# Performance work log

Hardware: AMD Instinct MI355X
Metric: run time of the kernel (lower is better)

The kernel has to match this reference:

```python
import jax, jax.numpy as jnp
import numpy as np
import math

D_MODEL = 1024
N_HEADS = 16
HEAD_DIM = 64


def setup_inputs() -> dict:
    key = jax.random.key(0)
    k_x, k_q, k_k, k_v, k_o = jax.random.split(key, 5)
    lecun = jax.nn.initializers.lecun_normal()
    return {
        "x": jax.random.normal(k_x, (4, 2048, D_MODEL), dtype=jnp.float32),
        "W_q": lecun(k_q, (N_HEADS, D_MODEL, HEAD_DIM), jnp.float32),
        "W_k": lecun(k_k, (N_HEADS, D_MODEL, HEAD_DIM), jnp.float32),
        "W_v": lecun(k_v, (N_HEADS, D_MODEL, HEAD_DIM), jnp.float32),
        "W_o": lecun(k_o, (D_MODEL, D_MODEL), jnp.float32),
    }


def reference(x, W_q, W_k, W_v, W_o):
    # x: [b, l, e]; W_{q,k,v}: [h, e, d]; W_o: [e, e]
    q = jnp.einsum('ble,hed->bhld', x, W_q)
    k = jnp.einsum('ble,hed->bhld', x, W_k)
    v = jnp.einsum('ble,hed->bhld', x, W_v)
    scores = jnp.einsum('bhld,bhsd->bhls', q, k) / math.sqrt(HEAD_DIM)
    attn = jax.nn.softmax(scores, axis=-1)
    av = jnp.einsum('bhls,bhsd->bhld', attn, v)  # [b, h, l, d]
    b, h, l, d = av.shape
    concat = jnp.transpose(av, (0, 2, 1, 3)).reshape(b, l, h * d)
    out = jnp.einsum('ble,eo->blo', concat, W_o)
    return jnp.asarray(out, dtype=jnp.float32)
```

## Files before the change

kernel.cpp:

```cpp
#include <hip/hip_runtime.h>

#define BATCH 4
#define LSEQ  2048
#define DM    1024
#define NH    16
#define HD    64
#define NTOK  (BATCH * LSEQ)

typedef _Float16 f16x8 __attribute__((ext_vector_type(8)));
typedef _Float16 f16x4 __attribute__((ext_vector_type(4)));
typedef __fp16   hf16x2 __attribute__((ext_vector_type(2)));
typedef float    f32x4 __attribute__((ext_vector_type(4)));

typedef __attribute__((address_space(1))) const unsigned int GU32;
typedef __attribute__((address_space(3))) unsigned int LU32;

__device__ __forceinline__ void gload_lds16(const _Float16* g, _Float16* l)
{
    __builtin_amdgcn_global_load_lds(
        (GU32*)(unsigned long long)g,
        (LU32*)(unsigned int)(unsigned long long)l, 16, 0, 0);
}


__global__ __launch_bounds__(256) void cvt_kernel(const float* __restrict__ src,
                                                  _Float16* __restrict__ dst, int n4)
{
    int i = blockIdx.x * 256 + threadIdx.x;
    if (i >= n4) return;
    float4 v = ((const float4*)src)[i];
    f16x4 h;
    h[0] = (_Float16)v.x; h[1] = (_Float16)v.y; h[2] = (_Float16)v.z; h[3] = (_Float16)v.w;
    ((f16x4*)dst)[i] = h;
}

__global__ __launch_bounds__(256) void tconv3_kernel(
    const float* __restrict__ Wq, const float* __restrict__ Wk,
    const float* __restrict__ Wv, _Float16* __restrict__ dst)
{
    const int z = blockIdx.z;
    const int which = z >> 4, h = z & 15;
    const float* __restrict__ src =
        ((which == 0) ? Wq : (which == 1) ? Wk : Wv) + (size_t)h * DM * HD;
    _Float16* __restrict__ d = dst + (size_t)z * DM * HD;
    const int e0 = blockIdx.y * 64;
    __shared__ float Ls[64][65];
    const int t = threadIdx.x;
    #pragma unroll
    for (int j = 0; j < 4; ++j) {
        int cidx = t + j * 256;
        int row = cidx >> 4, col4 = (cidx & 15) * 4;
        float4 v = *(const float4*)&src[(size_t)(e0 + row) * HD + col4];
        Ls[row][col4] = v.x; Ls[row][col4+1] = v.y; Ls[row][col4+2] = v.z; Ls[row][col4+3] = v.w;
    }
    __syncthreads();
    const int dd = t & 63, sc = t >> 6;
    alignas(16) _Float16 tmp[16];
    #pragma unroll
    for (int i = 0; i < 16; ++i) tmp[i] = (_Float16)Ls[sc * 16 + i][dd];
    *(f16x8*)&d[(size_t)dd * DM + e0 + sc * 16]     = *(f16x8*)&tmp[0];
    *(f16x8*)&d[(size_t)dd * DM + e0 + sc * 16 + 8] = *(f16x8*)&tmp[8];
}

__global__ __launch_bounds__(256) void tconv_kernel(const float* __restrict__ src,
                                                    _Float16* __restrict__ dst, int E, int D)
{
    const int d0 = blockIdx.x * 64, e0 = blockIdx.y * 64;
    __shared__ float Ls[64][65];
    const int t = threadIdx.x;
    #pragma unroll
    for (int j = 0; j < 4; ++j) {
        int cidx = t + j * 256;
        int row = cidx >> 4, col4 = (cidx & 15) * 4;
        float4 v = *(const float4*)&src[(size_t)(e0 + row) * D + d0 + col4];
        Ls[row][col4] = v.x; Ls[row][col4+1] = v.y; Ls[row][col4+2] = v.z; Ls[row][col4+3] = v.w;
    }
    __syncthreads();
    const int dd = t & 63, sc = t >> 6;
    alignas(16) _Float16 tmp[16];
    #pragma unroll
    for (int i = 0; i < 16; ++i) tmp[i] = (_Float16)Ls[sc * 16 + i][dd];
    *(f16x8*)&dst[(size_t)(d0 + dd) * E + e0 + sc * 16]     = *(f16x8*)&tmp[0];
    *(f16x8*)&dst[(size_t)(d0 + dd) * E + e0 + sc * 16 + 8] = *(f16x8*)&tmp[8];
}

template<int MODE>
__global__ __launch_bounds__(256) void gemm_kernel(
    const _Float16* __restrict__ A, const _Float16* __restrict__ B,
    float* __restrict__ out32,
    _Float16* __restrict__ qo, _Float16* __restrict__ ko, _Float16* __restrict__ vto)
{
    const int n0 = blockIdx.x * 128, m0 = blockIdx.y * 128;
    __shared__ _Float16 As[128 * 64];
    __shared__ _Float16 Bs[128 * 64];
    const int t = threadIdx.x;
    const int lane = t & 63, w = t >> 6;
    const int quad = lane >> 4, c = lane & 15;
    const int wm = (w & 1) * 64, wn = (w >> 1) * 64;
    const int srow = lane >> 3;
    const int scol8 = ((lane & 7) ^ (lane >> 3)) * 8;

    const int colsw = (quad ^ (c & 7)) * 8;
    const _Float16* Ap0 = &As[(wm + c) * 64 + colsw];
    const _Float16* Ap1 = &As[(wm + c) * 64 + (colsw ^ 32)];
    const _Float16* Bp0 = &Bs[(wn + c) * 64 + colsw];
    const _Float16* Bp1 = &Bs[(wn + c) * 64 + (colsw ^ 32)];

    f32x4 acc[4][4];
    #pragma unroll
    for (int i = 0; i < 4; ++i)
        #pragma unroll
        for (int j = 0; j < 4; ++j) acc[i][j] = {0.f, 0.f, 0.f, 0.f};

    for (int e0 = 0; e0 < DM; e0 += 64) {
        __syncthreads();
        #pragma unroll
        for (int j = 0; j < 4; ++j) {
            int ch = w * 4 + j;
            gload_lds16(A + (size_t)(m0 + ch * 8 + srow) * DM + e0 + scol8, As + ch * 512);
            gload_lds16(B + (size_t)(n0 + ch * 8 + srow) * DM + e0 + scol8, Bs + ch * 512);
        }
        __syncthreads();
        #pragma unroll
        for (int kc = 0; kc < 2; ++kc) {
            const _Float16* Ap = kc ? Ap1 : Ap0;
            const _Float16* Bp = kc ? Bp1 : Bp0;
            f16x8 af[4], bf[4];
            #pragma unroll
            for (int mt = 0; mt < 4; ++mt) af[mt] = *(const f16x8*)(Ap + mt * 1024);
            #pragma unroll
            for (int nt = 0; nt < 4; ++nt) bf[nt] = *(const f16x8*)(Bp + nt * 1024);
            #pragma unroll
            for (int mt = 0; mt < 4; ++mt)
                #pragma unroll
                for (int nt = 0; nt < 4; ++nt)
                    acc[mt][nt] = __builtin_amdgcn_mfma_f32_16x16x32_f16(af[mt], bf[nt], acc[mt][nt], 0, 0, 0);
        }
    }

    if (MODE == 0) {
        #pragma unroll
        for (int mt = 0; mt < 4; ++mt)
            #pragma unroll
            for (int nt = 0; nt < 4; ++nt)
                #pragma unroll
                for (int r = 0; r < 4; ++r) {
                    int row = m0 + wm + mt * 16 + quad * 4 + r;
                    int col = n0 + wn + nt * 16 + c;
                    out32[(size_t)row * DM + col] = acc[mt][nt][r];
                }
    } else {
        const int mi = (n0 + wn) >> 6;
        const int which = mi >> 4, hh = mi & 15;
        if (which == 2) {
            #pragma unroll
            for (int mt = 0; mt < 4; ++mt) {
                int tok0 = m0 + wm + mt * 16 + quad * 4;
                int b = tok0 >> 11, l = tok0 & (LSEQ - 1);
                #pragma unroll
                for (int nt = 0; nt < 4; ++nt) {
                    int d = nt * 16 + c;
                    f16x4 pk;
                    pk[0] = (_Float16)acc[mt][nt][0];
                    pk[1] = (_Float16)acc[mt][nt][1];
                    pk[2] = (_Float16)acc[mt][nt][2];
                    pk[3] = (_Float16)acc[mt][nt][3];
                    *(f16x4*)&vto[((size_t)(b * NH + hh) * HD + d) * LSEQ + l] = pk;
                }
            }
        } else {
            _Float16* dst = (which == 0) ? qo : ko;
            const float vs = (which == 0) ? 0.18033688011112042f : 1.0f;
            #pragma unroll
            for (int mt = 0; mt < 4; ++mt)
                #pragma unroll
                for (int nt = 0; nt < 4; ++nt)
                    #pragma unroll
                    for (int r = 0; r < 4; ++r) {
                        int tok = m0 + wm + mt * 16 + quad * 4 + r;
                        int b = tok >> 11, l = tok & (LSEQ - 1);
                        int d = nt * 16 + c;
                        dst[((size_t)(b * NH + hh) * LSEQ + l) * HD + d] = (_Float16)(acc[mt][nt][r] * vs);
                    }
        }
    }
}

__global__ __launch_bounds__(256, 3) void attn_kernel(
    const _Float16* __restrict__ Qg, const _Float16* __restrict__ Kg,
    const _Float16* __restrict__ Vtg, _Float16* __restrict__ concat)
{
    const int bh = blockIdx.x;
    const int q0 = blockIdx.y * 128;
    const int b = bh >> 4, h = bh & (NH - 1);
    __shared__ _Float16 Ks[2][64 * 64];
    __shared__ _Float16 Vts[2][64 * 64];
    __shared__ _Float16 Ps[4][32][72];
    const int t = threadIdx.x;
    const int lane = t & 63, w = t >> 6;
    const int quad = lane >> 4, c = lane & 15;
    const int srow = lane >> 3;
    const int scol8 = ((lane & 7) ^ (lane >> 3)) * 8;

    const int colsw = (quad ^ (c & 7)) * 8;
    const int kOffA = c * 64 + colsw;
    const int kOffB = c * 64 + (colsw ^ 32);
    _Float16*       PsW = &Ps[w][c][quad * 4];
    const _Float16* PsR = &Ps[w][c][quad * 8];

    f16x8 qf[2][2];
    #pragma unroll
    for (int mi = 0; mi < 2; ++mi)
        #pragma unroll
        for (int kc = 0; kc < 2; ++kc)
            qf[mi][kc] = *(const f16x8*)&Qg[((size_t)bh * LSEQ + q0 + w * 32 + mi * 16 + c) * HD + kc * 32 + quad * 8];

    f32x4 o[2][4];
    #pragma unroll
    for (int mi = 0; mi < 2; ++mi)
        #pragma unroll
        for (int dt = 0; dt < 4; ++dt) o[mi][dt] = {0.f, 0.f, 0.f, 0.f};
    float lp[2] = {0.f, 0.f};

    auto stage = [&](int bi, int s0n) {
        #pragma unroll
        for (int j = 0; j < 2; ++j) {
            int ch = w * 2 + j;
            gload_lds16(Kg  + ((size_t)bh * LSEQ + s0n + ch * 8 + srow) * HD + scol8, &Ks[bi][ch * 512]);
            gload_lds16(Vtg + ((size_t)bh * HD + ch * 8 + srow) * LSEQ + s0n + scol8, &Vts[bi][ch * 512]);
        }
    };

    constexpr int NT = LSEQ / 64;
    stage(0, 0);
    int cur = 0;

    for (int tt = 0; tt < NT; ++tt) {
        if (tt + 1 < NT) {
            stage(cur ^ 1, (tt + 1) * 64);
            asm volatile("s_waitcnt vmcnt(4)" ::: "memory");
        } else {
            asm volatile("s_waitcnt vmcnt(0)" ::: "memory");
        }
        __builtin_amdgcn_s_barrier();
        __builtin_amdgcn_sched_barrier(0);

        const _Float16* Kb = &Ks[cur][0];
        const _Float16* Vb = &Vts[cur][0];

        #pragma unroll
        for (int st = 0; st < 4; ++st) {
            f32x4 sT[2];
            #pragma unroll
            for (int mi = 0; mi < 2; ++mi) sT[mi] = {0.f, 0.f, 0.f, 0.f};
            #pragma unroll
            for (int kc = 0; kc < 2; ++kc) {
                f16x8 kf = *(const f16x8*)(Kb + (kc ? kOffB : kOffA) + st * 1024);
                #pragma unroll
                for (int mi = 0; mi < 2; ++mi)
                    sT[mi] = __builtin_amdgcn_mfma_f32_16x16x32_f16(kf, qf[mi][kc], sT[mi], 0, 0, 0);
            }
            #pragma unroll
            for (int mi = 0; mi < 2; ++mi) {
                float p0 = __builtin_amdgcn_exp2f(sT[mi][0]);
                float p1 = __builtin_amdgcn_exp2f(sT[mi][1]);
                float p2 = __builtin_amdgcn_exp2f(sT[mi][2]);
                float p3 = __builtin_amdgcn_exp2f(sT[mi][3]);
                lp[mi] += (p0 + p1) + (p2 + p3);
                union { hf16x2 h2[2]; f16x4 h4; } u;
                u.h2[0] = __builtin_amdgcn_cvt_pkrtz(p0, p1);
                u.h2[1] = __builtin_amdgcn_cvt_pkrtz(p2, p3);
                *(f16x4*)(PsW + mi * 1152 + st * 16) = u.h4;
            }
        }

        #pragma unroll
        for (int sc = 0; sc < 2; ++sc) {
            f16x8 pf[2];
            #pragma unroll
            for (int mi = 0; mi < 2; ++mi)
                pf[mi] = *(const f16x8*)(PsR + mi * 1152 + sc * 32);
            #pragma unroll
            for (int dt = 0; dt < 4; ++dt) {
                f16x8 vf = *(const f16x8*)(Vb + (sc ? kOffB : kOffA) + dt * 1024);
                #pragma unroll
                for (int mi = 0; mi < 2; ++mi)
                    o[mi][dt] = __builtin_amdgcn_mfma_f32_16x16x32_f16(pf[mi], vf, o[mi][dt], 0, 0, 0);
            }
        }

        __builtin_amdgcn_s_barrier();
        cur ^= 1;
    }

    #pragma unroll
    for (int mi = 0; mi < 2; ++mi) {
        lp[mi] += __shfl_xor(lp[mi], 16);
        lp[mi] += __shfl_xor(lp[mi], 32);
    }

    #pragma unroll
    for (int mi = 0; mi < 2; ++mi)
        #pragma unroll
        for (int r = 0; r < 4; ++r) {
            float inv = 1.f / __shfl(lp[mi], quad * 4 + r);
            int row = q0 + w * 32 + mi * 16 + quad * 4 + r;
            #pragma unroll
            for (int dt = 0; dt < 4; ++dt)
                concat[((size_t)b * LSEQ + row) * DM + h * HD + dt * 16 + c] =
                    (_Float16)(o[mi][dt][r] * inv);
        }
}

extern "C" void kernel_launch(void* const* d_in, const int* in_sizes, int n_in,
                              void* d_out, int out_size, void* d_ws, size_t ws_size,
                              hipStream_t stream)
{
    (void)in_sizes; (void)n_in; (void)out_size; (void)ws_size;

    const float* x  = (const float*)d_in[0];
    const float* Wq = (const float*)d_in[1];
    const float* Wk = (const float*)d_in[2];
    const float* Wv = (const float*)d_in[3];
    const float* Wo = (const float*)d_in[4];
    float* out = (float*)d_out;

    const size_t XE = (size_t)NTOK * DM;
    const size_t WQKV = (size_t)3 * NH * HD * DM;
    _Float16* xh  = (_Float16*)d_ws;
    _Float16* WtA = xh + XE;
    _Float16* Wot = WtA + WQKV;
    _Float16* q   = Wot + (size_t)DM * DM;
    _Float16* k   = q + XE;
    _Float16* vt  = k + XE;
    _Float16* cc  = vt + XE;

    cvt_kernel<<<8192, 256, 0, stream>>>(x, xh, (int)(XE / 4));
    tconv3_kernel<<<dim3(1, 16, 48), 256, 0, stream>>>(Wq, Wk, Wv, WtA);
    tconv_kernel<<<dim3(16, 16, 1), 256, 0, stream>>>(Wo, Wot, DM, DM);

    gemm_kernel<1><<<dim3(24, 64), 256, 0, stream>>>(xh, WtA, nullptr, q, k, vt);
    attn_kernel<<<dim3(64, LSEQ / 128), 256, 0, stream>>>(q, k, vt, cc);
    gemm_kernel<0><<<dim3(8, 64), 256, 0, stream>>>(cc, Wot, out, nullptr, nullptr, nullptr);
}
```

Before: 280.2 us.

## Switch attention to 32x32x16 MFMA and keep P in registers

```diff
diff --git a/kernel.cpp b/kernel.cpp
--- a/kernel.cpp
+++ b/kernel.cpp
@@ -11,6 +11,7 @@
 typedef _Float16 f16x4 __attribute__((ext_vector_type(4)));
 typedef __fp16   hf16x2 __attribute__((ext_vector_type(2)));
 typedef float    f32x4 __attribute__((ext_vector_type(4)));
+typedef float    f32x16 __attribute__((ext_vector_type(16)));
 
 typedef __attribute__((address_space(1))) const unsigned int GU32;
 typedef __attribute__((address_space(3))) unsigned int LU32;
@@ -186,41 +187,30 @@
     }
 }
 
-__global__ __launch_bounds__(256, 3) void attn_kernel(
+__global__ __launch_bounds__(256, 4) void attn_kernel(
     const _Float16* __restrict__ Qg, const _Float16* __restrict__ Kg,
     const _Float16* __restrict__ Vtg, _Float16* __restrict__ concat)
 {
     const int bh = blockIdx.x;
     const int q0 = blockIdx.y * 128;
-    const int b = bh >> 4, h = bh & (NH - 1);
+    const int b = bh >> 4, head = bh & (NH - 1);
     __shared__ _Float16 Ks[2][64 * 64];
     __shared__ _Float16 Vts[2][64 * 64];
-    __shared__ _Float16 Ps[4][32][72];
     const int t = threadIdx.x;
     const int lane = t & 63, w = t >> 6;
-    const int quad = lane >> 4, c = lane & 15;
+    const int m = lane & 31, hl = lane >> 5;
     const int srow = lane >> 3;
     const int scol8 = ((lane & 7) ^ (lane >> 3)) * 8;
 
-    const int colsw = (quad ^ (c & 7)) * 8;
-    const int kOffA = c * 64 + colsw;
-    const int kOffB = c * 64 + (colsw ^ 32);
-    _Float16*       PsW = &Ps[w][c][quad * 4];
-    const _Float16* PsR = &Ps[w][c][quad * 8];
-
-    f16x8 qf[2][2];
-    #pragma unroll
-    for (int mi = 0; mi < 2; ++mi)
-        #pragma unroll
-        for (int kc = 0; kc < 2; ++kc)
-            qf[mi][kc] = *(const f16x8*)&Qg[((size_t)bh * LSEQ + q0 + w * 32 + mi * 16 + c) * HD + kc * 32 + quad * 8];
-
-    f32x4 o[2][4];
-    #pragma unroll
-    for (int mi = 0; mi < 2; ++mi)
-        #pragma unroll
-        for (int dt = 0; dt < 4; ++dt) o[mi][dt] = {0.f, 0.f, 0.f, 0.f};
-    float lp[2] = {0.f, 0.f};
+    f16x8 qf[4];
+    #pragma unroll
+    for (int kstep = 0; kstep < 4; ++kstep)
+        qf[kstep] = *(const f16x8*)&Qg[((size_t)bh * LSEQ + q0 + w * 32 + m) * HD + kstep * 16 + hl * 8];
+
+    f32x16 o[2];
+    #pragma unroll
+    for (int i = 0; i < 16; ++i) { o[0][i] = 0.f; o[1][i] = 0.f; }
+    float lp = 0.f;
 
     auto stage = [&](int bi, int s0n) {
         #pragma unroll
@@ -248,68 +238,65 @@
         const _Float16* Kb = &Ks[cur][0];
         const _Float16* Vb = &Vts[cur][0];
 
-        #pragma unroll
-        for (int st = 0; st < 4; ++st) {
-            f32x4 sT[2];
-            #pragma unroll
-            for (int mi = 0; mi < 2; ++mi) sT[mi] = {0.f, 0.f, 0.f, 0.f};
-            #pragma unroll
-            for (int kc = 0; kc < 2; ++kc) {
-                f16x8 kf = *(const f16x8*)(Kb + (kc ? kOffB : kOffA) + st * 1024);
-                #pragma unroll
-                for (int mi = 0; mi < 2; ++mi)
-                    sT[mi] = __builtin_amdgcn_mfma_f32_16x16x32_f16(kf, qf[mi][kc], sT[mi], 0, 0, 0);
+        f16x8 pf[4];
+        #pragma unroll
+        for (int sblk = 0; sblk < 2; ++sblk) {
+            const int rr = sblk * 32 + m;
+            const int rx = rr & 7;
+            const _Float16* Krow = Kb + rr * 64;
+            f32x16 sT;
+            #pragma unroll
+            for (int i = 0; i < 16; ++i) sT[i] = 0.f;
+            #pragma unroll
+            for (int kstep = 0; kstep < 4; ++kstep) {
+                f16x8 kf = *(const f16x8*)(Krow + (((kstep * 2 + hl) ^ rx) * 8));
+                sT = __builtin_amdgcn_mfma_f32_32x32x16_f16(kf, qf[kstep], sT, 0, 0, 0);
             }
-            #pragma unroll
-            for (int mi = 0; mi < 2; ++mi) {
-                float p0 = __builtin_amdgcn_exp2f(sT[mi][0]);
-                float p1 = __builtin_amdgcn_exp2f(sT[mi][1]);
-                float p2 = __builtin_amdgcn_exp2f(sT[mi][2]);
-                float p3 = __builtin_amdgcn_exp2f(sT[mi][3]);
-                lp[mi] += (p0 + p1) + (p2 + p3);
-                union { hf16x2 h2[2]; f16x4 h4; } u;
-                u.h2[0] = __builtin_amdgcn_cvt_pkrtz(p0, p1);
-                u.h2[1] = __builtin_amdgcn_cvt_pkrtz(p2, p3);
-                *(f16x4*)(PsW + mi * 1152 + st * 16) = u.h4;
+            union { unsigned int u[4]; f16x8 v; } P0, P1;
+            #pragma unroll
+            for (int q = 0; q < 8; ++q) {
+                float e0 = __builtin_amdgcn_exp2f(sT[2 * q]);
+                float e1 = __builtin_amdgcn_exp2f(sT[2 * q + 1]);
+                lp += e0 + e1;
+                union { hf16x2 h; unsigned int u; } uu;
+                uu.h = __builtin_amdgcn_cvt_pkrtz(e0, e1);
+                if (q < 4) P0.u[q] = uu.u; else P1.u[q - 4] = uu.u;
             }
-        }
-
-        #pragma unroll
-        for (int sc = 0; sc < 2; ++sc) {
-            f16x8 pf[2];
-            #pragma unroll
-            for (int mi = 0; mi < 2; ++mi)
-                pf[mi] = *(const f16x8*)(PsR + mi * 1152 + sc * 32);
-            #pragma unroll
-            for (int dt = 0; dt < 4; ++dt) {
-                f16x8 vf = *(const f16x8*)(Vb + (sc ? kOffB : kOffA) + dt * 1024);
-                #pragma unroll
-                for (int mi = 0; mi < 2; ++mi)
-                    o[mi][dt] = __builtin_amdgcn_mfma_f32_16x16x32_f16(pf[mi], vf, o[mi][dt], 0, 0, 0);
+            pf[sblk * 2 + 0] = P0.v;
+            pf[sblk * 2 + 1] = P1.v;
+        }
+
+        #pragma unroll
+        for (int dblk = 0; dblk < 2; ++dblk) {
+            const int dd = dblk * 32 + m;
+            const int dx = dd & 7;
+            const _Float16* Vrow = Vb + dd * 64;
+            #pragma unroll
+            for (int sstep = 0; sstep < 4; ++sstep) {
+                union { f16x4 h4[2]; f16x8 v; } vv;
+                vv.h4[0] = *(const f16x4*)(Vrow + (((2 * sstep    ) ^ dx) * 8) + hl * 4);
+                vv.h4[1] = *(const f16x4*)(Vrow + (((2 * sstep + 1) ^ dx) * 8) + hl * 4);
+                o[dblk] = __builtin_amdgcn_mfma_f32_32x32x16_f16(pf[sstep], vv.v, o[dblk], 0, 0, 0);
             }
         }
 
+        asm volatile("s_waitcnt lgkmcnt(0)" ::: "memory");
         __builtin_amdgcn_s_barrier();
         cur ^= 1;
     }
 
-    #pragma unroll
-    for (int mi = 0; mi < 2; ++mi) {
-        lp[mi] += __shfl_xor(lp[mi], 16);
-        lp[mi] += __shfl_xor(lp[mi], 32);
-    }
-
-    #pragma unroll
-    for (int mi = 0; mi < 2; ++mi)
-        #pragma unroll
-        for (int r = 0; r < 4; ++r) {
-            float inv = 1.f / __shfl(lp[mi], quad * 4 + r);
-            int row = q0 + w * 32 + mi * 16 + quad * 4 + r;
-            #pragma unroll
-            for (int dt = 0; dt < 4; ++dt)
-                concat[((size_t)b * LSEQ + row) * DM + h * HD + dt * 16 + c] =
-                    (_Float16)(o[mi][dt][r] * inv);
-        }
+    lp += __shfl_xor(lp, 32);
+
+    #pragma unroll
+    for (int rg = 0; rg < 16; ++rg) {
+        const int mrow = (rg & 3) + 8 * (rg >> 2) + 4 * hl;
+        const float inv = 1.f / __shfl(lp, mrow);
+        const int row = q0 + w * 32 + mrow;
+        #pragma unroll
+        for (int dblk = 0; dblk < 2; ++dblk)
+            concat[((size_t)b * LSEQ + row) * DM + head * HD + dblk * 32 + m] =
+                (_Float16)(o[dblk][rg] * inv);
+    }
 }
 
 extern "C" void kernel_launch(void* const* d_in, const int* in_sizes, int n_in,
```

Result: no change. 284.1 us (+1.4%).
